# Kernel optimization log

Measured on AMD Instinct MI355X. Metric: run time of the kernel, lower is better.

The kernel has to match this reference:

```python
import jax, jax.numpy as jnp
import numpy as np

B, N, FH, H, FO = 8, 1024, 128, 8, 64
FIN = 2 * FH  # f_hid * 2
NEG = -1e9
SLOPE = 0.2  # leaky_relu negative slope (GAT default)


def setup_inputs() -> dict:
    key = jax.random.key(0)
    ks = jax.random.split(key, 10)
    x = jax.random.normal(ks[0], (B, FIN), jnp.float32)
    A = jax.random.randint(ks[1], (B, N, N), 0, 2, jnp.int32)  # 0/1 dense adjacency
    mask_zero = jnp.ones((B, N, 1), jnp.float32)  # node validity mask
    p_atten = jax.random.uniform(ks[2], (B, N), jnp.float32)  # unused in forward body
    e_atten = jax.random.uniform(ks[3], (B, N, FIN), jnp.float32)
    Npost = jax.random.normal(ks[4], (N, FIN), jnp.float32) * np.float32(1.0 / np.sqrt(FIN))  # kaiming-ish
    w = jax.random.normal(ks[5], (H, FIN, FO), jnp.float32) * np.float32(1.0 / np.sqrt(FIN))
    a_src = jax.random.normal(ks[6], (H, FO), jnp.float32) * np.float32(0.1)
    a_dst = jax.random.normal(ks[7], (H, FO), jnp.float32) * np.float32(0.1)
    bias = jnp.zeros((FO,), jnp.float32)
    return {"x": x, "A": A, "mask_zero": mask_zero, "p_atten": p_atten,
            "e_atten": e_atten, "Npost": Npost, "w": w, "a_src": a_src,
            "a_dst": a_dst, "bias": bias}


def reference(x, A, mask_zero, p_atten, e_atten, Npost, w, a_src, a_dst, bias):
    # broadcast-mul feature gating: x [B,FIN] repeated over N posts, gated by Npost*e_atten
    recx = x[:, None, :] * (Npost[None, :, :] * e_atten)          # [B,N,FIN]
    # BatchGAT (DeepInf-style multi-head graph attention, dropout disabled / eval mode)
    h = jnp.einsum('bnf,hfo->bhno', recx, w)                      # [B,H,N,FO]
    s = jnp.einsum('bhno,ho->bhn', h, a_src)                      # src attention term
    d = jnp.einsum('bhno,ho->bhn', h, a_dst)                      # dst attention term
    logits = jax.nn.leaky_relu(s[:, :, :, None] + d[:, :, None, :], SLOPE)  # [B,H,N,N]
    adj = (A > 0)[:, None, :, :]                                  # [B,1,N,N]
    logits = jnp.where(adj, logits, NEG)
    attn = jax.nn.softmax(logits, axis=-1)                        # masked row softmax
    out = jnp.einsum('bhnm,bhmo->bhno', attn, h) + bias           # aggregate neighbors
    out = out.mean(axis=1)                                        # average heads -> [B,N,FO]
    return out * mask_zero                                        # zero padded nodes
```

## Files before the change

kernel.cpp:

```cpp
#include <hip/hip_runtime.h>

typedef __attribute__((ext_vector_type(8))) short          bf16x8;
typedef __attribute__((ext_vector_type(8))) unsigned short u16x8;
typedef __attribute__((ext_vector_type(4))) unsigned short u16x4;
typedef __attribute__((ext_vector_type(4))) float          f32x4;
typedef __attribute__((ext_vector_type(4))) unsigned int   u32x4;

union U8 { u16x8 u; bf16x8 b; u32x4 w; };
union U4 { u16x4 u; unsigned w[2]; };

__device__ __forceinline__ unsigned short f2bf(float f){
  unsigned u = __float_as_uint(f);
  return (unsigned short)((u + 0x7fffu + ((u >> 16) & 1u)) >> 16);
}
__device__ __forceinline__ unsigned pack_bf16(float lo, float hi){
  unsigned a = __float_as_uint(hi) + 0x8000u;
  unsigned b = __float_as_uint(lo) + 0x8000u;
  return __builtin_amdgcn_perm(a, b, 0x07060302u);
}
__device__ __forceinline__ unsigned maskpack(float e0, float e1, unsigned m){
  unsigned r;
  asm("v_cvt_pk_bf16_f32 %0, %1, %2" : "=v"(r) : "v"(e0), "v"(e1));
  return r & m;
}

#define NN  1024
#define FIN 256
#define NH  8
#define FO  64

__global__ __launch_bounds__(256) void stage0(
    const float* __restrict__ w, const int* __restrict__ A,
    const float* __restrict__ bias, const float* __restrict__ mz,
    unsigned short* __restrict__ wfrag, unsigned long long* __restrict__ Abits,
    float* __restrict__ out)
{
  const int tid = blockIdx.x * 256 + threadIdx.x;
  if (tid < 16384){
    const int lane = tid & 63, ss = (tid >> 6) & 3, kc = (tid >> 8) & 7, h = tid >> 11;
    const int o = 16 * ss + (lane & 15);
    const int f = kc * 32 + (lane >> 4) * 8;
    u16x8 r;
    #pragma unroll
    for (int j = 0; j < 8; j++) r[j] = f2bf(w[(h * FIN + f + j) * FO + o]);
    *(u16x8*)(wfrag + tid * 8) = r;
  }
  #pragma unroll
  for (int k = 0; k < 2; k++){
    const int i = tid + k * 262144;
    out[i] = bias[i & 63] * mz[i >> 6];
  }
  for (int i = tid; i < 8388608; i += 262144){
    unsigned long long m = __ballot(A[i] > 0);
    if ((threadIdx.x & 63) == 0) Abits[i >> 6] = m;
  }
}

__global__ __launch_bounds__(512, 4) void stageA(
    const float* __restrict__ x, const float* __restrict__ e_at,
    const float* __restrict__ Np, const unsigned short* __restrict__ wfrag,
    const float* __restrict__ a_src, const float* __restrict__ a_dst,
    unsigned short* __restrict__ hT,
    float* __restrict__ Rt, float* __restrict__ expd, float* __restrict__ expd2)
{
  __shared__ unsigned short rex[16 * 264];
  const int t = threadIdx.x;
  const int n0 = blockIdx.x * 16, b = blockIdx.y;

  {
    const int row = t >> 5, f0 = (t & 31) * 8;
    const int nrow = n0 + row;
    const float* ep = e_at + (b * NN + nrow) * FIN + f0;
    const float* qp = Np + nrow * FIN + f0;
    const float* xp = x + b * FIN + f0;
    f32x4 e0 = *(const f32x4*)ep, e1 = *(const f32x4*)(ep + 4);
    f32x4 q0 = *(const f32x4*)qp, q1 = *(const f32x4*)(qp + 4);
    f32x4 x0 = *(const f32x4*)xp, x1 = *(const f32x4*)(xp + 4);
    u16x8 r;
    #pragma unroll
    for (int j = 0; j < 4; j++){
      r[j]     = f2bf(e0[j] * q0[j] * x0[j]);
      r[j + 4] = f2bf(e1[j] * q1[j] * x1[j]);
    }
    *(u16x8*)(rex + row * 264 + f0) = r;
  }
  __syncthreads();

  const int h = t >> 6, lane = t & 63, quad = lane >> 4, l15 = lane & 15;
  const unsigned short* wf = wfrag + h * 16384 + lane * 8;

  f32x4 acc[4] = {};
  #pragma unroll
  for (int kc = 0; kc < 8; kc++){
    U8 a0, bf[4];
    a0.u = *(const u16x8*)(rex + l15 * 264 + kc * 32 + quad * 8);
    #pragma unroll
    for (int ss = 0; ss < 4; ss++) bf[ss].u = *(const u16x8*)(wf + (kc * 4 + ss) * 512);
    #pragma unroll
    for (int ss = 0; ss < 4; ss++)
      acc[ss] = __builtin_amdgcn_mfma_f32_16x16x32_bf16(a0.b, bf[ss].b, acc[ss], 0, 0, 0);
  }

  {
    const int mtile = blockIdx.x >> 1, moff = (blockIdx.x & 1) * 16;
    unsigned short* pan = hT + (size_t)(((b * NH + h) * 32 + mtile) * 64) * 32;
    #pragma unroll
    for (int ss = 0; ss < 4; ss++){
      U4 v;
      v.w[0] = pack_bf16(acc[ss][0], acc[ss][1]);
      v.w[1] = pack_bf16(acc[ss][2], acc[ss][3]);
      *(u16x4*)(pan + (16 * ss + l15) * 32 + moff + quad * 4) = v.u;
    }
  }

  float as4[4], ad4[4];
  #pragma unroll
  for (int ss = 0; ss < 4; ss++){
    as4[ss] = a_src[h * FO + 16 * ss + l15];
    ad4[ss] = a_dst[h * FO + 16 * ss + l15];
  }
  #pragma unroll
  for (int i = 0; i < 4; i++){
    float ps = 0.f, pd = 0.f;
    #pragma unroll
    for (int ss = 0; ss < 4; ss++){ ps += acc[ss][i] * as4[ss]; pd += acc[ss][i] * ad4[ss]; }
    #pragma unroll
    for (int off = 1; off < 16; off <<= 1){
      ps += __shfl_xor(ps, off);
      pd += __shfl_xor(pd, off);
    }
    if (l15 == 0){
      const int idx = (b * NH + h) * NN + n0 + quad * 4 + i;
      Rt[idx]    = __expf(0.8f * ps);
      expd[idx]  = __expf(pd);
      expd2[idx] = __expf(0.2f * pd);
    }
  }
}

__global__ __launch_bounds__(256, 4) void stageB(
    const unsigned* __restrict__ Aw,
    const unsigned short* __restrict__ hT,
    const float* __restrict__ Rt,
    const float* __restrict__ expd, const float* __restrict__ expd2,
    const float* __restrict__ mz, float* __restrict__ out)
{
  __shared__ float ed_l[2 * NN];
  __shared__ float e2_l[2 * NN];
  __shared__ unsigned mask_l[32 * 33];
  __shared__ __align__(8) unsigned lut[16][2];
  __shared__ float l_l[4 * 16];

  const int fid = blockIdx.x;
  const int gb = (fid & 7) * 128 + (fid >> 3);
  const int n0 = (gb & 31) * 32, hq = (gb >> 5) & 3, b = gb >> 7;

  const int t = threadIdx.x;
  const int w = t >> 6, lane = t & 63, quad = lane >> 4, l15 = lane & 15;
  const int hl = w & 1, mh = w >> 1;
  const int h = hq * 2 + hl;

  if (t < 64) l_l[t] = 0.f;
  if (t < 16){
    lut[t][0] = (t & 1 ? 0xFFFFu : 0u) | (t & 2 ? 0xFFFF0000u : 0u);
    lut[t][1] = (t & 4 ? 0xFFFFu : 0u) | (t & 8 ? 0xFFFF0000u : 0u);
  }
  {
    const float* s1 = expd  + (b * NH + hq * 2) * NN;
    const float* s2 = expd2 + (b * NH + hq * 2) * NN;
    *(f32x4*)(ed_l + t * 8)     = *(const f32x4*)(s1 + t * 8);
    *(f32x4*)(ed_l + t * 8 + 4) = *(const f32x4*)(s1 + t * 8 + 4);
    *(f32x4*)(e2_l + t * 8)     = *(const f32x4*)(s2 + t * 8);
    *(f32x4*)(e2_l + t * 8 + 4) = *(const f32x4*)(s2 + t * 8 + 4);
  }
  #pragma unroll
  for (int k = 0; k < 4; k++){
    const int i = t + k * 256;
    mask_l[(i >> 5) * 33 + (i & 31)] = Aw[(b * NN + n0 + (i >> 5)) * 32 + (i & 31)];
  }
  __syncthreads();

  const int hb = (b * NH + h) * NN;
  const float Rv0 = Rt[hb + n0 + l15];
  const float Rv1 = Rt[hb + n0 + 16 + l15];
  const unsigned short* pb = hT + (size_t)(b * NH + h) * 65536 + l15 * 32 + quad * 8;
  const float* edh = ed_l + hl * NN + quad * 8;
  const float* e2h = e2_l + hl * NN + quad * 8;
  const int c0 = mh * 16;
  const int qs = quad * 8;

  U8 pan[4];
  #pragma unroll
  for (int ss = 0; ss < 4; ss++)
    pan[ss].u = *(const u16x8*)(pb + (size_t)c0 * 2048 + ss * 512);
  unsigned mw0 = mask_l[l15 * 33 + c0];
  unsigned mw1 = mask_l[(16 + l15) * 33 + c0];

  U8 ones;
  #pragma unroll
  for (int j = 0; j < 8; j++) ones.u[j] = 0x3F80;

  f32x4 acc0[4] = {}, acc1[4] = {};
  f32x4 accl0 = {}, accl1 = {};

  for (int cc = 0; cc < 16; cc++){
    const int c = c0 + cc;
    const unsigned am0 = (mw0 >> qs) & 0xFF;
    const unsigned am1 = (mw1 >> qs) & 0xFF;
    const uint2 la0 = *(const uint2*)&lut[am0 & 15][0];
    const uint2 lb0 = *(const uint2*)&lut[(am0 >> 4) & 15][0];
    const uint2 la1 = *(const uint2*)&lut[am1 & 15][0];
    const uint2 lb1 = *(const uint2*)&lut[(am1 >> 4) & 15][0];
    if (cc + 1 < 16){
      mw0 = mask_l[l15 * 33 + c + 1];
      mw1 = mask_l[(16 + l15) * 33 + c + 1];
    }
    const f32x4 d01 = *(const f32x4*)(edh + c * 32);
    const f32x4 d23 = *(const f32x4*)(edh + c * 32 + 4);
    const f32x4 g01 = *(const f32x4*)(e2h + c * 32);
    const f32x4 g23 = *(const f32x4*)(e2h + c * 32 + 4);
    {
      const f32x4 p01 = Rv0 * d01, p23 = Rv0 * d23;
      U8 p;
      p.w[0] = maskpack(fmaxf(p01[0], g01[0]), fmaxf(p01[1], g01[1]), la0.x);
      p.w[1] = maskpack(fmaxf(p01[2], g01[2]), fmaxf(p01[3], g01[3]), la0.y);
      p.w[2] = maskpack(fmaxf(p23[0], g23[0]), fmaxf(p23[1], g23[1]), lb0.x);
      p.w[3] = maskpack(fmaxf(p23[2], g23[2]), fmaxf(p23[3], g23[3]), lb0.y);
      #pragma unroll
      for (int ss = 0; ss < 4; ss++)
        acc0[ss] = __builtin_amdgcn_mfma_f32_16x16x32_bf16(p.b, pan[ss].b, acc0[ss], 0, 0, 0);
      accl0 = __builtin_amdgcn_mfma_f32_16x16x32_bf16(p.b, ones.b, accl0, 0, 0, 0);
    }
    {
      const f32x4 p01 = Rv1 * d01, p23 = Rv1 * d23;
      U8 p;
      p.w[0] = maskpack(fmaxf(p01[0], g01[0]), fmaxf(p01[1], g01[1]), la1.x);
      p.w[1] = maskpack(fmaxf(p01[2], g01[2]), fmaxf(p01[3], g01[3]), la1.y);
      p.w[2] = maskpack(fmaxf(p23[0], g23[0]), fmaxf(p23[1], g23[1]), lb1.x);
      p.w[3] = maskpack(fmaxf(p23[2], g23[2]), fmaxf(p23[3], g23[3]), lb1.y);
      #pragma unroll
      for (int ss = 0; ss < 4; ss++)
        acc1[ss] = __builtin_amdgcn_mfma_f32_16x16x32_bf16(p.b, pan[ss].b, acc1[ss], 0, 0, 0);
      accl1 = __builtin_amdgcn_mfma_f32_16x16x32_bf16(p.b, ones.b, accl1, 0, 0, 0);
    }
    if (cc + 1 < 16){
      #pragma unroll
      for (int ss = 0; ss < 4; ss++)
        pan[ss].u = *(const u16x8*)(pb + (size_t)(c + 1) * 2048 + ss * 512);
    }
  }

  if (l15 == 0){
    #pragma unroll
    for (int i = 0; i < 4; i++){
      atomicAdd(&l_l[(hl * 2 + 0) * 16 + quad * 4 + i], accl0[i]);
      atomicAdd(&l_l[(hl * 2 + 1) * 16 + quad * 4 + i], accl1[i]);
    }
  }
  __syncthreads();

  const float* mzp = mz + b * NN + n0;
  #pragma unroll
  for (int i = 0; i < 4; i++){
    const int r16 = quad * 4 + i;
    const float invm0 = (0.125f / l_l[(hl * 2 + 0) * 16 + r16]) * mzp[r16];
    const float invm1 = (0.125f / l_l[(hl * 2 + 1) * 16 + r16]) * mzp[16 + r16];
    float* op0 = out + (size_t)(b * NN + n0 + r16) * FO + l15;
    float* op1 = out + (size_t)(b * NN + n0 + 16 + r16) * FO + l15;
    #pragma unroll
    for (int ss = 0; ss < 4; ss++){
      atomicAdd(op0 + ss * 16, acc0[ss][i] * invm0);
      atomicAdd(op1 + ss * 16, acc1[ss][i] * invm1);
    }
  }
}

extern "C" void kernel_launch(void* const* d_in, const int* in_sizes, int n_in,
                              void* d_out, int out_size, void* d_ws, size_t ws_size,
                              hipStream_t stream)
{
  (void)in_sizes; (void)n_in; (void)out_size; (void)ws_size;
  const float* x    = (const float*)d_in[0];
  const int*   A    = (const int*)d_in[1];
  const float* mz   = (const float*)d_in[2];
  const float* e_at = (const float*)d_in[4];
  const float* Np   = (const float*)d_in[5];
  const float* w    = (const float*)d_in[6];
  const float* asrc = (const float*)d_in[7];
  const float* adst = (const float*)d_in[8];
  const float* bias = (const float*)d_in[9];
  float* out = (float*)d_out;

  char* ws = (char*)d_ws;
  unsigned short* wfrag = (unsigned short*)ws;
  unsigned short* hT    = (unsigned short*)(ws + 262144);
  float* Rt    = (float*)(ws + 8650752);
  float* expd  = (float*)(ws + 8912896);
  float* expd2 = (float*)(ws + 9175040);
  unsigned long long* Abits = (unsigned long long*)(ws + 9437184);

  stage0<<<dim3(1024), dim3(256), 0, stream>>>(w, A, bias, mz, wfrag, Abits, out);
  stageA<<<dim3(64, 8), dim3(512), 0, stream>>>(x, e_at, Np, wfrag, asrc, adst,
                                                hT, Rt, expd, expd2);
  stageB<<<dim3(1024), dim3(256), 0, stream>>>((const unsigned*)Abits, hT,
                                               Rt, expd, expd2, mz, out);
}
```

Before: 158.0 us.

## Split stageB per head, reduce key-chunk work per block, merge outputs in LDS

stageB now assigns one head per block and splits each block's 32 key chunks across 4 waves of 8 chunks, doubling the grid to 2048 blocks and raising the launch-bounds occupancy target. The mask words are read straight from global memory, and the expd tables share one smaller LDS buffer, which cuts LDS use per block. Partial outputs from the waves are first summed in LDS and then written with one global atomic per element, which reduces global atomic traffic per block. The cost is more blocks overall, each redoing setup loads, a per-head global atomic merge across the 8 heads, and extra barriers.

```diff
diff --git a/kernel.cpp b/kernel.cpp
--- a/kernel.cpp
+++ b/kernel.cpp
@@ -138,45 +138,35 @@
   }
 }
 
-__global__ __launch_bounds__(256, 4) void stageB(
+__global__ __launch_bounds__(256, 8) void stageB(
     const unsigned* __restrict__ Aw,
     const unsigned short* __restrict__ hT,
     const float* __restrict__ Rt,
     const float* __restrict__ expd, const float* __restrict__ expd2,
     const float* __restrict__ mz, float* __restrict__ out)
 {
-  __shared__ float ed_l[2 * NN];
-  __shared__ float e2_l[2 * NN];
-  __shared__ unsigned mask_l[32 * 33];
+  __shared__ float tab[2112];
   __shared__ __align__(8) unsigned lut[16][2];
-  __shared__ float l_l[4 * 16];
+  __shared__ float l_l[32];
 
   const int fid = blockIdx.x;
-  const int gb = (fid & 7) * 128 + (fid >> 3);
-  const int n0 = (gb & 31) * 32, hq = (gb >> 5) & 3, b = gb >> 7;
+  const int b = fid & 7, h = (fid >> 3) & 7, nt = fid >> 6;
+  const int n0 = nt * 32;
 
   const int t = threadIdx.x;
   const int w = t >> 6, lane = t & 63, quad = lane >> 4, l15 = lane & 15;
-  const int hl = w & 1, mh = w >> 1;
-  const int h = hq * 2 + hl;
-
-  if (t < 64) l_l[t] = 0.f;
+  const int mh = w;
+
+  if (t < 32) l_l[t] = 0.f;
   if (t < 16){
     lut[t][0] = (t & 1 ? 0xFFFFu : 0u) | (t & 2 ? 0xFFFF0000u : 0u);
     lut[t][1] = (t & 4 ? 0xFFFFu : 0u) | (t & 8 ? 0xFFFF0000u : 0u);
   }
   {
-    const float* s1 = expd  + (b * NH + hq * 2) * NN;
-    const float* s2 = expd2 + (b * NH + hq * 2) * NN;
-    *(f32x4*)(ed_l + t * 8)     = *(const f32x4*)(s1 + t * 8);
-    *(f32x4*)(ed_l + t * 8 + 4) = *(const f32x4*)(s1 + t * 8 + 4);
-    *(f32x4*)(e2_l + t * 8)     = *(const f32x4*)(s2 + t * 8);
-    *(f32x4*)(e2_l + t * 8 + 4) = *(const f32x4*)(s2 + t * 8 + 4);
-  }
-  #pragma unroll
-  for (int k = 0; k < 4; k++){
-    const int i = t + k * 256;
-    mask_l[(i >> 5) * 33 + (i & 31)] = Aw[(b * NN + n0 + (i >> 5)) * 32 + (i & 31)];
+    const float* s1 = expd  + (b * NH + h) * NN;
+    const float* s2 = expd2 + (b * NH + h) * NN;
+    *(f32x4*)(tab + t * 4)        = *(const f32x4*)(s1 + t * 4);
+    *(f32x4*)(tab + 1024 + t * 4) = *(const f32x4*)(s2 + t * 4);
   }
   __syncthreads();
 
@@ -184,17 +174,18 @@
   const float Rv0 = Rt[hb + n0 + l15];
   const float Rv1 = Rt[hb + n0 + 16 + l15];
   const unsigned short* pb = hT + (size_t)(b * NH + h) * 65536 + l15 * 32 + quad * 8;
-  const float* edh = ed_l + hl * NN + quad * 8;
-  const float* e2h = e2_l + hl * NN + quad * 8;
-  const int c0 = mh * 16;
+  const float* edh = tab + quad * 8;
+  const float* e2h = tab + 1024 + quad * 8;
+  const unsigned* awp = Aw + (b * NN + n0) * 32;
+  const int c0 = mh * 8;
   const int qs = quad * 8;
 
   U8 pan[4];
   #pragma unroll
   for (int ss = 0; ss < 4; ss++)
     pan[ss].u = *(const u16x8*)(pb + (size_t)c0 * 2048 + ss * 512);
-  unsigned mw0 = mask_l[l15 * 33 + c0];
-  unsigned mw1 = mask_l[(16 + l15) * 33 + c0];
+  unsigned mw0 = awp[l15 * 32 + c0];
+  unsigned mw1 = awp[(16 + l15) * 32 + c0];
 
   U8 ones;
   #pragma unroll
@@ -203,7 +194,7 @@
   f32x4 acc0[4] = {}, acc1[4] = {};
   f32x4 accl0 = {}, accl1 = {};
 
-  for (int cc = 0; cc < 16; cc++){
+  for (int cc = 0; cc < 8; cc++){
     const int c = c0 + cc;
     const unsigned am0 = (mw0 >> qs) & 0xFF;
     const unsigned am1 = (mw1 >> qs) & 0xFF;
@@ -211,9 +202,9 @@
     const uint2 lb0 = *(const uint2*)&lut[(am0 >> 4) & 15][0];
     const uint2 la1 = *(const uint2*)&lut[am1 & 15][0];
     const uint2 lb1 = *(const uint2*)&lut[(am1 >> 4) & 15][0];
-    if (cc + 1 < 16){
-      mw0 = mask_l[l15 * 33 + c + 1];
-      mw1 = mask_l[(16 + l15) * 33 + c + 1];
+    if (cc + 1 < 8){
+      mw0 = awp[l15 * 32 + c + 1];
+      mw1 = awp[(16 + l15) * 32 + c + 1];
     }
     const f32x4 d01 = *(const f32x4*)(edh + c * 32);
     const f32x4 d23 = *(const f32x4*)(edh + c * 32 + 4);
@@ -243,7 +234,7 @@
         acc1[ss] = __builtin_amdgcn_mfma_f32_16x16x32_bf16(p.b, pan[ss].b, acc1[ss], 0, 0, 0);
       accl1 = __builtin_amdgcn_mfma_f32_16x16x32_bf16(p.b, ones.b, accl1, 0, 0, 0);
     }
-    if (cc + 1 < 16){
+    if (cc + 1 < 8){
       #pragma unroll
       for (int ss = 0; ss < 4; ss++)
         pan[ss].u = *(const u16x8*)(pb + (size_t)(c + 1) * 2048 + ss * 512);
@@ -253,25 +244,35 @@
   if (l15 == 0){
     #pragma unroll
     for (int i = 0; i < 4; i++){
-      atomicAdd(&l_l[(hl * 2 + 0) * 16 + quad * 4 + i], accl0[i]);
-      atomicAdd(&l_l[(hl * 2 + 1) * 16 + quad * 4 + i], accl1[i]);
-    }
-  }
-  __syncthreads();
-
-  const float* mzp = mz + b * NN + n0;
+      atomicAdd(&l_l[quad * 4 + i], accl0[i]);
+      atomicAdd(&l_l[16 + quad * 4 + i], accl1[i]);
+    }
+  }
+  __syncthreads();
+
+  for (int i = t; i < 2080; i += 256) tab[i] = 0.f;
+  __syncthreads();
+
   #pragma unroll
   for (int i = 0; i < 4; i++){
-    const int r16 = quad * 4 + i;
-    const float invm0 = (0.125f / l_l[(hl * 2 + 0) * 16 + r16]) * mzp[r16];
-    const float invm1 = (0.125f / l_l[(hl * 2 + 1) * 16 + r16]) * mzp[16 + r16];
-    float* op0 = out + (size_t)(b * NN + n0 + r16) * FO + l15;
-    float* op1 = out + (size_t)(b * NN + n0 + 16 + r16) * FO + l15;
+    const int r0 = quad * 4 + i;
+    const float ia = 1.0f / l_l[r0];
+    const float ib = 1.0f / l_l[16 + r0];
     #pragma unroll
     for (int ss = 0; ss < 4; ss++){
-      atomicAdd(op0 + ss * 16, acc0[ss][i] * invm0);
-      atomicAdd(op1 + ss * 16, acc1[ss][i] * invm1);
-    }
+      atomicAdd(&tab[r0 * 65 + ss * 16 + l15], acc0[ss][i] * ia);
+      atomicAdd(&tab[(16 + r0) * 65 + ss * 16 + l15], acc1[ss][i] * ib);
+    }
+  }
+  __syncthreads();
+
+  {
+    const int r = t >> 3;
+    const float sc = 0.125f * mz[b * NN + n0 + r];
+    float* op = out + (size_t)(b * NN + n0 + r) * FO + (t & 7) * 8;
+    const float* mrg = tab + r * 65 + (t & 7) * 8;
+    #pragma unroll
+    for (int k = 0; k < 8; k++) atomicAdd(op + k, mrg[k] * sc);
   }
 }
 
@@ -302,6 +303,6 @@
   stage0<<<dim3(1024), dim3(256), 0, stream>>>(w, A, bias, mz, wfrag, Abits, out);
   stageA<<<dim3(64, 8), dim3(512), 0, stream>>>(x, e_at, Np, wfrag, asrc, adst,
                                                 hT, Rt, expd, expd2);
-  stageB<<<dim3(1024), dim3(256), 0, stream>>>((const unsigned*)Abits, hT,
+  stageB<<<dim3(2048), dim3(256), 0, stream>>>((const unsigned*)Abits, hT,
                                                Rt, expd, expd2, mz, out);
 }
```

Result: slower. 325.8 us (+106.2%).
